# Performance work log

Hardware: AMD Instinct MI355X
Metric: run time of the kernel (lower is better)

Reference implementation:

```python
import jax, jax.numpy as jnp
import numpy as np
from jax import lax

B, D = 512, 64
LOWER, UPPER = -10.0, 10.0
TOL = 1e-6
MAX_ITER = 200
EXPAND = 2.0


def setup_inputs() -> dict:
    key = jax.random.key(0)
    kw, ka, ky = jax.random.split(key, 3)
    W = jnp.tril(jax.random.normal(kw, (D, D), dtype=jnp.float32), -1) * jnp.float32(1.0 / np.sqrt(D))
    a = jax.random.uniform(ka, (D,), dtype=jnp.float32, minval=0.5, maxval=1.5)
    y = jax.random.normal(ky, (B, D), dtype=jnp.float32) * 1.5
    return {"y": y, "a": a, "W": W}


def _transform(x, a, W):
    return jax.nn.softplus(a) * x + jnp.tanh(x) @ W.T


def _adapt_interval(func, lower, upper):
    # faithful port of adapt_interval_to_include_root (incl. sign evaluation at
    # pre-update bounds, exactly as in the original body_fn)
    fl, fu = func(lower), func(upper)

    def cond(s):
        lo, up, e, sl, su, it = s
        return jnp.logical_and(sl == su, it < MAX_ITER)

    def body(s):
        lo, up, e, sl, su, it = s
        new_lo = jnp.where(sl == 1, lo - e, up)
        new_up = jnp.where(sl == 1, lo, up + e)
        return (new_lo, new_up, e * EXPAND, jnp.sign(func(lo)), jnp.sign(func(up)), it + 1)

    init = (jnp.float32(lower), jnp.float32(upper), jnp.float32(upper - lower), jnp.sign(fl), jnp.sign(fu), 0)
    lo, up, _, _, _, _ = lax.while_loop(cond, body, init)
    return lo, up


def _bisection(func):
    lo, up = _adapt_interval(func, LOWER, UPPER)

    def cond(s):
        lo, up, it = s
        return jnp.logical_and(up - lo > 2 * TOL, it < MAX_ITER)

    def body(s):
        lo, up, it = s
        mid = (lo + up) / 2
        pos = func(mid) >= 0
        return (jnp.where(pos, lo, mid), jnp.where(pos, mid, up), it + 1)

    lo, up, _ = lax.while_loop(cond, body, (lo, up, 0))
    return (lo + up) / 2


def _invert_one(y_vec, a, W):
    def scan_fn(carry, _):
        x, i = carry

        def scalar_fn(xi):
            return _transform(x.at[i].set(xi), a, W)[i] - y_vec[i]

        root = _bisection(scalar_fn)
        return (x.at[i].set(root), i + 1), None

    init = (jnp.full(D, (LOWER + UPPER) / 2, dtype=y_vec.dtype), 0)
    (x, _), _ = lax.scan(scan_fn, init, None, length=D)
    return x


def reference(y, a, W):
    return jax.vmap(lambda yv: _invert_one(yv, a, W))(y)
```

## Files before the change

kernel.cpp:

```cpp
#include <hip/hip_runtime.h>


#define DD 64
#define LOWERB (-10.0f)
#define UPPERB (10.0f)

__device__ __forceinline__ float sgnf(float v) {
    return (v > 0.f) ? 1.f : ((v < 0.f) ? -1.f : 0.f);
}

__device__ __attribute__((noinline)) float bisect_fallback(float s, float cmy) {
    float lo = LOWERB, up = UPPERB, e = UPPERB - LOWERB;
    float sl = sgnf(fmaf(s, lo, cmy));
    float su = sgnf(fmaf(s, up, cmy));
    int it = 0;
    while (sl == su && it < 200) {
        float nlo = (sl == 1.f) ? (lo - e) : up;
        float nup = (sl == 1.f) ? lo : (up + e);
        float osl = sgnf(fmaf(s, lo, cmy));
        float osu = sgnf(fmaf(s, up, cmy));
        lo = nlo; up = nup; e *= 2.f; sl = osl; su = osu; ++it;
    }
    it = 0;
    while ((up - lo) > 2e-6f && it < 200) {
        float mid = 0.5f * (lo + up);
        bool pos = fmaf(s, mid, cmy) >= 0.f;
        if (pos) up = mid; else lo = mid;
        ++it;
    }
    return 0.5f * (lo + up);
}

__device__ __forceinline__ float rl(float v, int l) {
    return __int_as_float(__builtin_amdgcn_readlane(__float_as_int(v), l));
}

__global__ __launch_bounds__(256) void ar_invert_kernel(
    const float* __restrict__ y, const float* __restrict__ a,
    const float* __restrict__ W, float* __restrict__ out, int B)
{
    __shared__ float Wt[DD * (DD + 1)];
    for (int k = threadIdx.x; k < DD * DD; k += 256) {
        int i = k >> 6, j = k & 63;
        Wt[j * (DD + 1) + i] = W[k];
    }
    __syncthreads();

    const int lane = threadIdx.x & 63;
    const int row  = (int)((blockIdx.x * 256u + threadIdx.x) >> 6);
    if (row >= B) return;

    float yv = y[row * DD + lane];
    float av = a[lane];
    float s  = av + log1pf(expf(-av));
    float rs = 1.f / s;

    float c = 0.f;
    float x = 0.f;

    for (int j = 0; j < DD; ++j) {
        float cj  = rl(c, j);
        float yj  = rl(yv, j);
        float rsj = rl(rs, j);
        float r = (yj - cj) * rsj;

        float sj  = rl(s, j);
        float cmy = cj - yj;
        float flo = fmaf(sj, LOWERB, cmy);
        float fup = fmaf(sj, UPPERB, cmy);
        if (sgnf(flo) == sgnf(fup)) {
            r = bisect_fallback(sj, cmy);
        }

        float t = tanhf(r);
        if (lane == j) x = r;
        c = fmaf(Wt[j * (DD + 1) + lane], t, c);
    }

    out[row * DD + lane] = x;
}

extern "C" void kernel_launch(void* const* d_in, const int* in_sizes, int n_in,
                              void* d_out, int out_size, void* d_ws, size_t ws_size,
                              hipStream_t stream) {
    const float* y = (const float*)d_in[0];
    const float* a = (const float*)d_in[1];
    const float* W = (const float*)d_in[2];
    float* out = (float*)d_out;
    const int B = in_sizes[0] / DD;
    const int threads = 256;
    const int blocks = (B * DD + threads - 1) / threads;
    ar_invert_kernel<<<blocks, threads, 0, stream>>>(y, a, W, out, B);
}
```

Before: 70.40 us.

## Keep W rows in registers, fast tanh, and defer bisection fallback to a rare second pass

Each lane now loads its row of W directly into 64 registers, which removes the shared-memory transpose and the block-wide barrier. The per-step residual is kept as u = y - c, so the closed-form root is uj*rs. tanh is computed with a hardware exp2 and reciprocal instead of tanhf. The bisection check is hoisted out of the fully unrolled main loop into a flag, and the exact path is rerun only when some step needs bracketing. The risks are register pressure from 64 floats plus the unroll, and lower tanh accuracy.

```diff
diff --git a/kernel.cpp b/kernel.cpp
--- a/kernel.cpp
+++ b/kernel.cpp
@@ -4,9 +4,19 @@
 #define DD 64
 #define LOWERB (-10.0f)
 #define UPPERB (10.0f)
+#define K2 2.8853900817779268f
 
 __device__ __forceinline__ float sgnf(float v) {
     return (v > 0.f) ? 1.f : ((v < 0.f) ? -1.f : 0.f);
+}
+
+__device__ __forceinline__ float rl(float v, int l) {
+    return __int_as_float(__builtin_amdgcn_readlane(__float_as_int(v), l));
+}
+
+__device__ __forceinline__ float tanh_fast_arg(float r_times_k2) {
+    float e = __builtin_amdgcn_exp2f(r_times_k2);
+    return fmaf(-2.f, __builtin_amdgcn_rcpf(e + 1.f), 1.f);
 }
 
 __device__ __attribute__((noinline)) float bisect_fallback(float s, float cmy) {
@@ -31,50 +41,60 @@
     return 0.5f * (lo + up);
 }
 
-__device__ __forceinline__ float rl(float v, int l) {
-    return __int_as_float(__builtin_amdgcn_readlane(__float_as_int(v), l));
-}
-
 __global__ __launch_bounds__(256) void ar_invert_kernel(
     const float* __restrict__ y, const float* __restrict__ a,
     const float* __restrict__ W, float* __restrict__ out, int B)
 {
-    __shared__ float Wt[DD * (DD + 1)];
-    for (int k = threadIdx.x; k < DD * DD; k += 256) {
-        int i = k >> 6, j = k & 63;
-        Wt[j * (DD + 1) + i] = W[k];
-    }
-    __syncthreads();
-
     const int lane = threadIdx.x & 63;
     const int row  = (int)((blockIdx.x * 256u + threadIdx.x) >> 6);
     if (row >= B) return;
 
-    float yv = y[row * DD + lane];
+    float wr[DD];
+    const float4* w4 = (const float4*)(W + lane * DD);
+    #pragma unroll
+    for (int k = 0; k < DD / 4; ++k) {
+        float4 v = w4[k];
+        wr[4 * k + 0] = v.x; wr[4 * k + 1] = v.y;
+        wr[4 * k + 2] = v.z; wr[4 * k + 3] = v.w;
+    }
+
+    const float u0 = y[row * DD + lane];
+    float u = u0;
     float av = a[lane];
     float s  = av + log1pf(expf(-av));
-    float rs = 1.f / s;
+    float rs  = 1.f / s;
+    float rs2 = rs * K2;
 
-    float c = 0.f;
     float x = 0.f;
+    bool bad = false;
 
+    #pragma unroll
     for (int j = 0; j < DD; ++j) {
-        float cj  = rl(c, j);
-        float yj  = rl(yv, j);
-        float rsj = rl(rs, j);
-        float r = (yj - cj) * rsj;
+        float uj  = rl(u, j);
+        float sj  = rl(s, j);
+        float flo = fmaf(sj, LOWERB, -uj);
+        float fup = fmaf(sj, UPPERB, -uj);
+        bad = bad || (sgnf(flo) == sgnf(fup));
+        float r = uj * rl(rs, j);
+        float t = tanh_fast_arg(uj * rl(rs2, j));
+        if (lane == j) x = r;
+        u = fmaf(-wr[j], t, u);
+    }
 
-        float sj  = rl(s, j);
-        float cmy = cj - yj;
-        float flo = fmaf(sj, LOWERB, cmy);
-        float fup = fmaf(sj, UPPERB, cmy);
-        if (sgnf(flo) == sgnf(fup)) {
-            r = bisect_fallback(sj, cmy);
+    if (bad) {
+        u = u0; x = 0.f;
+        for (int j = 0; j < DD; ++j) {
+            float uj = rl(u, j);
+            float sj = rl(s, j);
+            float flo = fmaf(sj, LOWERB, -uj);
+            float fup = fmaf(sj, UPPERB, -uj);
+            float r;
+            if (sgnf(flo) == sgnf(fup)) r = bisect_fallback(sj, -uj);
+            else                        r = uj * rl(rs, j);
+            float t = tanhf(r);
+            if (lane == j) x = r;
+            u = fmaf(-wr[j], t, u);
         }
-
-        float t = tanhf(r);
-        if (lane == j) x = r;
-        c = fmaf(Wt[j * (DD + 1) + lane], t, c);
     }
 
     out[row * DD + lane] = x;
```

Result: faster. 67.26 us (-4.5%).
